# Kernel tuning notes

Measured on AMD Instinct MI355X. Metric: run time of the kernel, lower is better.

Reference implementation:

```python
import jax, jax.numpy as jnp
import numpy as np

B, T, D, H = 4, 2048, 1024, 16
HD = D // H  # 64
EPS = 1e-5


def setup_inputs() -> dict:
    key = jax.random.key(0)
    ks = jax.random.split(key, 8)
    s = 0.02
    return {
        "X": jax.random.normal(ks[0], (B, T, D), dtype=jnp.float32),
        # per-head projection weights stacked: [H, D, HD] (no bias, matches nn.Linear(bias=False))
        "Wq": jax.random.normal(ks[1], (H, D, HD), dtype=jnp.float32) * s,
        "Wk": jax.random.normal(ks[2], (H, D, HD), dtype=jnp.float32) * s,
        "Wv": jax.random.normal(ks[3], (H, D, HD), dtype=jnp.float32) * s,
        "ln1_g": jnp.ones((D,), jnp.float32),
        "ln1_b": jnp.zeros((D,), jnp.float32),
        "W1": jax.random.normal(ks[4], (D, 4 * D), dtype=jnp.float32) * s,
        "b1": jnp.zeros((4 * D,), jnp.float32),
        "W2": jax.random.normal(ks[5], (4 * D, D), dtype=jnp.float32) * s,
        "b2": jnp.zeros((D,), jnp.float32),
        "ln2_g": jnp.ones((D,), jnp.float32),
        "ln2_b": jnp.zeros((D,), jnp.float32),
    }


def _layer_norm(x, g, b):
    m = jnp.mean(x, axis=-1, keepdims=True)
    v = jnp.mean((x - m) ** 2, axis=-1, keepdims=True)
    return (x - m) / jnp.sqrt(v + EPS) * g + b


def reference(X, Wq, Wk, Wv, ln1_g, ln1_b, W1, b1, W2, b2, ln2_g, ln2_b):
    # multi-head causal self-attention (naive full-matrix, matching source)
    Q = jnp.einsum('btd,hde->bhte', X, Wq)
    K = jnp.einsum('btd,hde->bhte', X, Wk)
    V = jnp.einsum('btd,hde->bhte', X, Wv)
    scores = jnp.einsum('bhte,bhse->bhts', Q, K) / jnp.sqrt(jnp.float32(HD))
    causal = jnp.tril(jnp.ones((T, T), dtype=bool))
    scores = jnp.where(causal, scores, jnp.finfo(scores.dtype).min)
    attn = jax.nn.softmax(scores, axis=-1)
    Yh = jnp.einsum('bhts,bhse->bhte', attn, V)  # [B,H,T,HD]
    Y = jnp.transpose(Yh, (0, 2, 1, 3)).reshape(B, T, D)  # concat heads

    X1 = _layer_norm(Y + X, ln1_g, ln1_b)
    ff = jax.nn.relu(X1 @ W1 + b1) @ W2 + b2  # dropout inactive (eval)
    X2 = ff + X1
    return _layer_norm(X2, ln2_g, ln2_b)
```

## Files before the change

### kernel.cpp

```cpp
#include <hip/hip_runtime.h>
#include <cstdint>


typedef _Float16 f16x8 __attribute__((ext_vector_type(8)));
typedef _Float16 f16x4 __attribute__((ext_vector_type(4)));
typedef float    f32x4 __attribute__((ext_vector_type(4)));

#define DEVI __device__ __forceinline__

typedef __attribute__((address_space(1))) uint32_t gas1_u32;
typedef __attribute__((address_space(3))) uint32_t las3_u32;

DEVI void gl2lds16(const void* g, void* l) {
  __builtin_amdgcn_global_load_lds((gas1_u32*)(uintptr_t)g,
                                   (las3_u32*)(uintptr_t)l, 16, 0, 0);
}

#define FENCE_BAR                                                            \
  __builtin_amdgcn_sched_barrier(0xF);                                       \
  __builtin_amdgcn_s_barrier();                                              \
  __builtin_amdgcn_sched_barrier(0xF);

__global__ __launch_bounds__(256) void preprocess(
    const float* __restrict__ X, _Float16* __restrict__ Xh,
    const float* __restrict__ Wq, const float* __restrict__ Wk,
    const float* __restrict__ Wv, _Float16* __restrict__ Wqkv,
    const float* __restrict__ W1, _Float16* __restrict__ W1t,
    const float* __restrict__ W2, _Float16* __restrict__ W2t) {
  const int idx = blockIdx.x;
  const int tid = threadIdx.x;
  if (idx < 4096) {
    const int i = (idx * 256 + tid) * 8;
    float4 a = *(const float4*)&X[i];
    float4 b = *(const float4*)&X[i + 4];
    f16x8 o;
    o[0] = (_Float16)a.x; o[1] = (_Float16)a.y; o[2] = (_Float16)a.z; o[3] = (_Float16)a.w;
    o[4] = (_Float16)b.x; o[5] = (_Float16)b.y; o[6] = (_Float16)b.z; o[7] = (_Float16)b.w;
    *(f16x8*)&Xh[i] = o;
    return;
  }
  __shared__ _Float16 T[64 * 72];
  const float* src;
  _Float16* dst;
  int k0, rowbase, stride, dstK;
  float scale = 1.0f;
  if (idx < 4864) {
    const int j = idx - 4096;
    const int z = j >> 4;
    const int which = z >> 4;
    const int slice = z & 15;
    src = ((which == 0) ? Wq : (which == 1) ? Wk : Wv) + (size_t)slice * 65536;
    scale = (which == 0) ? 0.18033688011112042f : 1.0f;
    k0 = (j & 15) * 64;
    rowbase = which * 1024 + slice * 64;
    stride = 64; dstK = 1024; dst = Wqkv;
  } else if (idx < 5888) {
    const int j = idx - 4864;
    src = W1 + (j >> 4) * 64;
    k0 = (j & 15) * 64;
    rowbase = (j >> 4) * 64;
    stride = 4096; dstK = 1024; dst = W1t;
  } else {
    const int j = idx - 5888;
    src = W2 + (j >> 6) * 64;
    k0 = (j & 63) * 64;
    rowbase = (j >> 6) * 64;
    stride = 1024; dstK = 4096; dst = W2t;
  }
#pragma unroll
  for (int p = 0; p < 4; ++p) {
    int c = p * 256 + tid;
    int kl = c >> 4;
    int nl = (c & 15) * 4;
    float4 v = *(const float4*)&src[(size_t)(k0 + kl) * stride + nl];
    T[(nl + 0) * 72 + kl] = (_Float16)(v.x * scale);
    T[(nl + 1) * 72 + kl] = (_Float16)(v.y * scale);
    T[(nl + 2) * 72 + kl] = (_Float16)(v.z * scale);
    T[(nl + 3) * 72 + kl] = (_Float16)(v.w * scale);
  }
  __syncthreads();
#pragma unroll
  for (int p = 0; p < 2; ++p) {
    int c = p * 256 + tid;
    int nl = c >> 3;
    int kc = (c & 7) * 8;
    f16x8 vv = *(const f16x8*)&T[nl * 72 + kc];
    *(f16x8*)&dst[(size_t)(rowbase + nl) * dstK + k0 + kc] = vv;
  }
}

__global__ __launch_bounds__(256) void transpose_v(
    const _Float16* __restrict__ Vh, _Float16* __restrict__ Vt) {
  __shared__ _Float16 T[64 * 72];
  const int t0 = blockIdx.x * 64;
  const size_t hb = (size_t)blockIdx.y * (2048 * 64);
  const int tid = threadIdx.x;
#pragma unroll
  for (int it = 0; it < 2; ++it) {
    const int c = it * 256 + tid;
    const int tl = c >> 3;
    const int ec = (c & 7) * 8;
    *(f16x8*)&T[tl * 72 + ec] =
        *(const f16x8*)&Vh[hb + (size_t)(t0 + tl) * 64 + ec];
  }
  __syncthreads();
#pragma unroll
  for (int it = 0; it < 2; ++it) {
    const int c = it * 256 + tid;
    const int el = c >> 3;
    const int tc = (c & 7) * 8;
    f16x8 o;
#pragma unroll
    for (int jj = 0; jj < 8; ++jj) o[jj] = T[(tc + jj) * 72 + el];
    *(f16x8*)&Vt[hb + (size_t)el * 2048 + t0 + tc] = o;
  }
}

template <int MODE>
__global__ __launch_bounds__(512, 1) void gemm4(
    const _Float16* __restrict__ A, const _Float16* __restrict__ Bt,
    int K, int N, int nbx, int cpx,
    const float* __restrict__ bias, const _Float16* __restrict__ residH,
    _Float16* __restrict__ outH,
    _Float16* __restrict__ outQ, _Float16* __restrict__ outKp,
    _Float16* __restrict__ outV) {
  __shared__ _Float16 As[2][2][128 * 64];
  __shared__ _Float16 Bs[2][128 * 64];
  const int tid = threadIdx.x;
  const int lane = tid & 63;
  const int w = tid >> 6;
  const int wr = w >> 1, wc = w & 1;
  const int lr = lane & 15, g = lane >> 4;
  const int o = (blockIdx.x & 7) * cpx + (blockIdx.x >> 3);
  const int m0 = (o / nbx) * 256, n0 = (o % nbx) * 128;
  const int NT = K >> 6;

  const _Float16* Ab = A + (size_t)m0 * K;
  const _Float16* Bb = Bt + (size_t)n0 * K;

  f32x4 acc[4][4] = {};

  auto STG = [&](const _Float16* src, _Float16* dst) {
#pragma unroll
    for (int it = 0; it < 2; ++it) {
      const int c = it * 512 + tid;
      const int r = c >> 3;
      const int ts = (c & 7) ^ (r & 7);
      gl2lds16(src + (size_t)r * K + ts * 8, dst + c * 8);
    }
  };

  STG(Ab, &As[0][0][0]);
  STG(Ab + 128 * (size_t)K, &As[0][1][0]);
  STG(Bb, &Bs[0][0]);
  STG(Ab + 64, &As[1][0][0]);
  STG(Ab + 128 * (size_t)K + 64, &As[1][1][0]);
  STG(Bb + 64, &Bs[1][0]);
  asm volatile("s_waitcnt vmcnt(6)" ::: "memory");
  FENCE_BAR;

  f16x8 af[4][2], bfL[2][2], bfH[2][2];

  for (int t = 0; t < NT; ++t) {
    const int b = t & 1;
#pragma unroll
    for (int mf = 0; mf < 4; ++mf) {
      const int rl = (wr & 1) * 64 + mf * 16 + lr;
#pragma unroll
      for (int k2 = 0; k2 < 2; ++k2)
        af[mf][k2] = *(const f16x8*)&As[b][wr >> 1]
            [rl * 64 + (((k2 * 4 + g) ^ (rl & 7)) << 3)];
    }
#pragma unroll
    for (int nf = 0; nf < 2; ++nf) {
      const int rb = wc * 64 + nf * 16 + lr;
#pragma unroll
      for (int k2 = 0; k2 < 2; ++k2)
        bfL[nf][k2] = *(const f16x8*)&Bs[b]
            [rb * 64 + (((k2 * 4 + g) ^ (rb & 7)) << 3)];
    }
    FENCE_BAR;
    if (t + 2 < NT) {
      STG(Ab + (size_t)(t + 2) * 64, &As[b][0][0]);
      STG(Ab + 128 * (size_t)K + (size_t)(t + 2) * 64, &As[b][1][0]);
    }
#pragma unroll
    for (int nf = 0; nf < 2; ++nf) {
      const int rb = wc * 64 + (nf + 2) * 16 + lr;
#pragma unroll
      for (int k2 = 0; k2 < 2; ++k2)
        bfH[nf][k2] = *(const f16x8*)&Bs[b]
            [rb * 64 + (((k2 * 4 + g) ^ (rb & 7)) << 3)];
    }
    __builtin_amdgcn_s_setprio(1);
#pragma unroll
    for (int mf = 0; mf < 4; ++mf)
#pragma unroll
      for (int nf = 0; nf < 2; ++nf)
#pragma unroll
        for (int k2 = 0; k2 < 2; ++k2)
          acc[mf][nf] = __builtin_amdgcn_mfma_f32_16x16x32_f16(
              af[mf][k2], bfL[nf][k2], acc[mf][nf], 0, 0, 0);
    __builtin_amdgcn_s_setprio(0);
    FENCE_BAR;
    if (t + 2 < NT) STG(Bb + (size_t)(t + 2) * 64, &Bs[b][0]);
    __builtin_amdgcn_s_setprio(1);
#pragma unroll
    for (int mf = 0; mf < 4; ++mf)
#pragma unroll
      for (int nf = 0; nf < 2; ++nf)
#pragma unroll
        for (int k2 = 0; k2 < 2; ++k2)
          acc[mf][nf + 2] = __builtin_amdgcn_mfma_f32_16x16x32_f16(
              af[mf][k2], bfH[nf][k2], acc[mf][nf + 2], 0, 0, 0);
    __builtin_amdgcn_s_setprio(0);
    if (t == NT - 2) {
      asm volatile("s_waitcnt vmcnt(0)" ::: "memory");
    } else if (t < NT - 2) {
      asm volatile("s_waitcnt vmcnt(6)" ::: "memory");
    }
    FENCE_BAR;
  }

#pragma unroll
  for (int mf = 0; mf < 4; ++mf) {
#pragma unroll
    for (int nf = 0; nf < 4; ++nf) {
#pragma unroll
      for (int rr = 0; rr < 4; ++rr) {
        const int row = m0 + wr * 64 + mf * 16 + g * 4 + rr;
        const int col = n0 + wc * 64 + nf * 16 + lr;
        float v = acc[mf][nf][rr];
        if constexpr (MODE == 0) {
          const int qkv = col >> 10;
          const int h = (col >> 6) & 15;
          const int e = col & 63;
          const int bb = row >> 11;
          const int tt = row & 2047;
          const size_t idx = (((size_t)bb * 16 + h) * 2048 + tt) * 64 + e;
          const _Float16 hv = (_Float16)v;
          if (qkv == 0)      outQ[idx] = hv;
          else if (qkv == 1) outKp[idx] = hv;
          else               outV[idx] = hv;
        } else {
          outH[(size_t)row * N + col] = (_Float16)(
              v + bias[col] + (float)residH[(size_t)row * N + col]);
        }
      }
    }
  }
}

__global__ __launch_bounds__(512, 1) void gemm8_ffn1(
    const _Float16* __restrict__ A, const _Float16* __restrict__ Bt,
    int K, int N, int nbx, int cpx,
    const float* __restrict__ bias, _Float16* __restrict__ outH) {
  __shared__ _Float16 As[2][2][128 * 64];
  __shared__ _Float16 Bs[2][2][128 * 64];
  const int tid = threadIdx.x;
  const int lane = tid & 63;
  const int w = tid >> 6;
  const int wr = w >> 2, wc = w & 3;
  const int lr = lane & 15, g = lane >> 4;
  const int o = (blockIdx.x & 7) * cpx + (blockIdx.x >> 3);
  const int m0 = (o / nbx) * 256, n0 = (o % nbx) * 256;
  const int NT = K >> 6;

  const _Float16* Ab = A + (size_t)m0 * K;
  const _Float16* Bb = Bt + (size_t)n0 * K;

  f32x4 acc[8][4] = {};

  auto STG = [&](const _Float16* src, _Float16* dst) {
#pragma unroll
    for (int it = 0; it < 2; ++it) {
      const int c = it * 512 + tid;
      const int r = c >> 3;
      const int ts = (c & 7) ^ (r & 7);
      gl2lds16(src + (size_t)r * K + ts * 8, dst + c * 8);
    }
  };

  STG(Ab, &As[0][0][0]);
  STG(Ab + 128 * (size_t)K, &As[0][1][0]);
  STG(Bb, &Bs[0][0][0]);
  STG(Bb + 128 * (size_t)K, &Bs[0][1][0]);
  STG(Ab + 64, &As[1][0][0]);
  STG(Ab + 128 * (size_t)K + 64, &As[1][1][0]);
  STG(Bb + 64, &Bs[1][0][0]);
  asm volatile("s_waitcnt vmcnt(6)" ::: "memory");
  FENCE_BAR;

  f16x8 afA[4][2], afB[4][2], bfL[2][2], bfH[2][2];

#define LDA8_(af, MLO, buf)                                                  \
  _Pragma("unroll") for (int mf = 0; mf < 4; ++mf) {                         \
    const int rl = (MLO + mf) * 16 + lr;                                     \
    _Pragma("unroll") for (int k2 = 0; k2 < 2; ++k2)                         \
      af[mf][k2] = *(const f16x8*)&As[buf][wr][rl * 64 +                     \
                      (((k2 * 4 + g) ^ (rl & 7)) << 3)];                     \
  }
#define LDB8_(bf, NLO, buf)                                                  \
  _Pragma("unroll") for (int nf = 0; nf < 2; ++nf) {                         \
    const int rb = wc * 64 + (NLO + nf) * 16 + lr;                           \
    _Pragma("unroll") for (int k2 = 0; k2 < 2; ++k2)                         \
      bf[nf][k2] = *(const f16x8*)&Bs[buf][rb >> 7][(rb & 127) * 64 +        \
                      (((k2 * 4 + g) ^ (rb & 7)) << 3)];                     \
  }
#define MMA8_(af, bf, MB, NB)                                                \
  __builtin_amdgcn_s_setprio(1);                                             \
  _Pragma("unroll") for (int mf = 0; mf < 4; ++mf)                           \
  _Pragma("unroll") for (int nf = 0; nf < 2; ++nf)                           \
  _Pragma("unroll") for (int k2 = 0; k2 < 2; ++k2)                           \
    acc[(MB) + mf][(NB) + nf] = __builtin_amdgcn_mfma_f32_16x16x32_f16(      \
        af[mf][k2], bf[nf][k2], acc[(MB) + mf][(NB) + nf], 0, 0, 0);         \
  __builtin_amdgcn_s_setprio(0);

  for (int t = 0; t < NT; ++t) {
    const int cur = t & 1, nxt = cur ^ 1;
    LDA8_(afA, 0, cur);
    LDB8_(bfL, 0, cur);
    if (t + 1 < NT)
      STG(Bb + 128 * (size_t)K + (size_t)(t + 1) * 64, &Bs[nxt][1][0]);
    FENCE_BAR;
    MMA8_(afA, bfL, 0, 0);
    FENCE_BAR;
    LDA8_(afB, 4, cur);
    FENCE_BAR;
    MMA8_(afB, bfL, 4, 0);
    FENCE_BAR;
    LDB8_(bfH, 2, cur);
    if (t + 2 < NT) STG(Ab + (size_t)(t + 2) * 64, &As[cur][0][0]);
    FENCE_BAR;
    MMA8_(afA, bfH, 0, 2);
    FENCE_BAR;
    if (t + 2 < NT) {
      STG(Ab + 128 * (size_t)K + (size_t)(t + 2) * 64, &As[cur][1][0]);
      STG(Bb + (size_t)(t + 2) * 64, &Bs[cur][0][0]);
    }
    if (t == NT - 2) {
      asm volatile("s_waitcnt vmcnt(0)" ::: "memory");
    } else if (t < NT - 2) {
      asm volatile("s_waitcnt vmcnt(6)" ::: "memory");
    }
    FENCE_BAR;
    MMA8_(afB, bfH, 4, 2);
    FENCE_BAR;
  }
#undef LDA8_
#undef LDB8_
#undef MMA8_

#pragma unroll
  for (int mf = 0; mf < 8; ++mf) {
#pragma unroll
    for (int nf = 0; nf < 4; ++nf) {
#pragma unroll
      for (int rr = 0; rr < 4; ++rr) {
        const int row = m0 + wr * 128 + mf * 16 + g * 4 + rr;
        const int col = n0 + wc * 64 + nf * 16 + lr;
        float v = fmaxf(acc[mf][nf][rr] + bias[col], 0.0f);
        outH[(size_t)row * N + col] = (_Float16)v;
      }
    }
  }
}

__global__ __launch_bounds__(256, 2) void attn_fwd9(
    const _Float16* __restrict__ Qg, const _Float16* __restrict__ Kg,
    const _Float16* __restrict__ Vtg, _Float16* __restrict__ Yg) {
  __shared__ _Float16 Ksm[2][64 * 64];
  __shared__ _Float16 Vts[2][64 * 64];
  __shared__ _Float16 Psm[128 * 72];
  const int tid = threadIdx.x;
  const int lane = tid & 63;
  const int w = tid >> 6;
  const int lr = lane & 15, g = lane >> 4;

  const int bid = blockIdx.x;
  const int bh  = (bid & 7) * 8 + ((bid >> 3) & 7);
  const int p   = bid >> 6;
  const int qtA = p, qtB = 15 - p;
  const int njA = 2 * p + 2;
  const int ntot = 34;

  const size_t hbo = (size_t)bh * (2048 * 64);
  const _Float16* Qb = Qg + hbo;
  const _Float16* Kb = Kg + hbo;
  const _Float16* Vb = Vtg + hbo;
  _Float16* Yb = Yg + hbo;

  f16x8 qfA[2][2], qfB[2][2];
#pragma unroll
  for (int mi = 0; mi < 2; ++mi) {
    const int rA = qtA * 128 + mi * 64 + w * 16 + lr;
    const int rB = qtB * 128 + mi * 64 + w * 16 + lr;
#pragma unroll
    for (int ss = 0; ss < 2; ++ss) {
      qfA[mi][ss] = *(const f16x8*)&Qb[(size_t)rA * 64 + ss * 32 + g * 8];
      qfB[mi][ss] = *(const f16x8*)&Qb[(size_t)rB * 64 + ss * 32 + g * 8];
    }
  }

  f32x4 accYA[2][4] = {}, accYB[2][4] = {};
  f32x4 accLA[2] = {}, accLB[2] = {};

  f16x8 ones;
#pragma unroll
  for (int i = 0; i < 8; ++i) ones[i] = (_Float16)1.0f;

  auto TK0 = [&](int u) { return (u < njA ? u : u - njA) * 64; };

  auto STAGE = [&](int bufi, int tk0) {
#pragma unroll
    for (int it = 0; it < 2; ++it) {
      const int c = it * 256 + tid;
      const int r = c >> 3;
      const int ts = (c & 7) ^ (r & 7);
      gl2lds16(Kb + (size_t)(tk0 + r) * 64 + ts * 8, &Ksm[bufi][c * 8]);
      gl2lds16(Vb + (size_t)r * 2048 + tk0 + ts * 8, &Vts[bufi][c * 8]);
    }
  };

  auto BODY = [&](int bufi, int qbase, int tk0, const f16x8 (&qf)[2][2],
                  f32x4 (&accY)[2][4], f32x4 (&accL)[2]) {
    const _Float16* Ks = Ksm[bufi];
    const _Float16* Vs = Vts[bufi];
    const int qlo0 = qbase + w * 16;
    const int qlo1 = qbase + 64 + w * 16;
    const bool act0 = (tk0 <= qlo0 + 15);
    f16x8 kf[4][2];
#pragma unroll
    for (int ni = 0; ni < 4; ++ni) {
      const int row = ni * 16 + lr;
#pragma unroll
      for (int kk = 0; kk < 2; ++kk)
        kf[ni][kk] = *(const f16x8*)&Ks[row * 64 + (((kk * 4 + g) ^ (row & 7)) << 3)];
    }
    f32x4 s0[4] = {}, s1[4] = {};
    __builtin_amdgcn_s_setprio(1);
    if (act0) {
#pragma unroll
      for (int ni = 0; ni < 4; ++ni)
#pragma unroll
        for (int kk = 0; kk < 2; ++kk)
          s0[ni] = __builtin_amdgcn_mfma_f32_16x16x32_f16(kf[ni][kk], qf[0][kk], s0[ni], 0, 0, 0);
    }
#pragma unroll
    for (int ni = 0; ni < 4; ++ni)
#pragma unroll
      for (int kk = 0; kk < 2; ++kk)
        s1[ni] = __builtin_amdgcn_mfma_f32_16x16x32_f16(kf[ni][kk], qf[1][kk], s1[ni], 0, 0, 0);
    __builtin_amdgcn_s_setprio(0);
    if (act0 && tk0 + 63 > qlo0) {
      const int qa = qlo0 + lr;
#pragma unroll
      for (int ni = 0; ni < 4; ++ni)
#pragma unroll
        for (int r = 0; r < 4; ++r)
          if (tk0 + ni * 16 + g * 4 + r > qa) s0[ni][r] = -3.0e38f;
    }
    if (tk0 + 63 > qlo1) {
      const int qa = qlo1 + lr;
#pragma unroll
      for (int ni = 0; ni < 4; ++ni)
#pragma unroll
        for (int r = 0; r < 4; ++r)
          if (tk0 + ni * 16 + g * 4 + r > qa) s1[ni][r] = -3.0e38f;
    }
    const int prow0 = w * 16 + lr;
    const int prow1 = 64 + w * 16 + lr;
    if (act0) {
#pragma unroll
      for (int ni = 0; ni < 4; ++ni) {
        auto a = __builtin_amdgcn_cvt_pkrtz(__builtin_amdgcn_exp2f(s0[ni][0]),
                                            __builtin_amdgcn_exp2f(s0[ni][1]));
        auto b = __builtin_amdgcn_cvt_pkrtz(__builtin_amdgcn_exp2f(s0[ni][2]),
                                            __builtin_amdgcn_exp2f(s0[ni][3]));
        f16x4 pk4;
        pk4[0] = a[0]; pk4[1] = a[1]; pk4[2] = b[0]; pk4[3] = b[1];
        *(f16x4*)&Psm[prow0 * 72 + ni * 16 + g * 4] = pk4;
      }
    }
#pragma unroll
    for (int ni = 0; ni < 4; ++ni) {
      auto a = __builtin_amdgcn_cvt_pkrtz(__builtin_amdgcn_exp2f(s1[ni][0]),
                                          __builtin_amdgcn_exp2f(s1[ni][1]));
      auto b = __builtin_amdgcn_cvt_pkrtz(__builtin_amdgcn_exp2f(s1[ni][2]),
                                          __builtin_amdgcn_exp2f(s1[ni][3]));
      f16x4 pk4;
      pk4[0] = a[0]; pk4[1] = a[1]; pk4[2] = b[0]; pk4[3] = b[1];
      *(f16x4*)&Psm[prow1 * 72 + ni * 16 + g * 4] = pk4;
    }
    __builtin_amdgcn_s_setprio(1);
#pragma unroll
    for (int ss = 0; ss < 2; ++ss) {
      f16x8 pa0 = {};
      f16x8 pa1 = *(const f16x8*)&Psm[prow1 * 72 + ss * 32 + g * 8];
      if (act0) pa0 = *(const f16x8*)&Psm[prow0 * 72 + ss * 32 + g * 8];
      if (act0) accL[0] = __builtin_amdgcn_mfma_f32_16x16x32_f16(pa0, ones, accL[0], 0, 0, 0);
      accL[1] = __builtin_amdgcn_mfma_f32_16x16x32_f16(pa1, ones, accL[1], 0, 0, 0);
#pragma unroll
      for (int ne = 0; ne < 4; ++ne) {
        const int vrow = ne * 16 + lr;
        const f16x8 vbf = *(const f16x8*)&Vs[vrow * 64 + (((ss * 4 + g) ^ (vrow & 7)) << 3)];
        if (act0) accY[0][ne] = __builtin_amdgcn_mfma_f32_16x16x32_f16(pa0, vbf, accY[0][ne], 0, 0, 0);
        accY[1][ne] = __builtin_amdgcn_mfma_f32_16x16x32_f16(pa1, vbf, accY[1][ne], 0, 0, 0);
      }
    }
    __builtin_amdgcn_s_setprio(0);
  };

  STAGE(0, TK0(0));
  for (int u = 0; u < ntot; ++u) {
    asm volatile("s_waitcnt vmcnt(0)" ::: "memory");
    __builtin_amdgcn_s_barrier();
    __builtin_amdgcn_sched_barrier(0xF);
    const int cur = u & 1;
    if (u + 1 < ntot) STAGE(cur ^ 1, TK0(u + 1));
    if (u < njA) BODY(cur, qtA * 128, u * 64, qfA, accYA, accLA);
    else         BODY(cur, qtB * 128, (u - njA) * 64, qfB, accYB, accLB);
  }

#pragma unroll
  for (int mi = 0; mi < 2; ++mi)
#pragma unroll
    for (int r = 0; r < 4; ++r) {
      const float invA = 1.0f / accLA[mi][r];
      const float invB = 1.0f / accLB[mi][r];
      const int qaA = qtA * 128 + mi * 64 + w * 16 + g * 4 + r;
      const int qaB = qtB * 128 + mi * 64 + w * 16 + g * 4 + r;
#pragma unroll
      for (int ne = 0; ne < 4; ++ne) {
        Yb[(size_t)qaA * 64 + ne * 16 + lr] = (_Float16)(accYA[mi][ne][r] * invA);
        Yb[(size_t)qaB * 64 + ne * 16 + lr] = (_Float16)(accYB[mi][ne][r] * invB);
      }
    }
}

__global__ __launch_bounds__(256) void ln1_fused(
    const _Float16* __restrict__ Yh, const float* __restrict__ X,
    const float* __restrict__ gam, const float* __restrict__ bet,
    _Float16* __restrict__ X1h) {
  const int row = blockIdx.x;
  const int b = row >> 11, t = row & 2047;
  const int tid = threadIdx.x;
  const int d0 = tid * 4;
  const int h = d0 >> 6, e = d0 & 63;
  const f16x4 y4 = *(const f16x4*)&Yh[(((size_t)b * 16 + h) * 2048 + t) * 64 + e];
  const float4 x = *(const float4*)&X[(size_t)row * 1024 + d0];
  float v0 = (float)y4[0] + x.x, v1 = (float)y4[1] + x.y;
  float v2 = (float)y4[2] + x.z, v3 = (float)y4[3] + x.w;
  float s = v0 + v1 + v2 + v3;
  float q = v0 * v0 + v1 * v1 + v2 * v2 + v3 * v3;
  for (int off = 32; off; off >>= 1) { s += __shfl_xor(s, off); q += __shfl_xor(q, off); }
  __shared__ float red[8];
  const int w = tid >> 6;
  if ((tid & 63) == 0) { red[w] = s; red[4 + w] = q; }
  __syncthreads();
  s = red[0] + red[1] + red[2] + red[3];
  q = red[4] + red[5] + red[6] + red[7];
  const float mean = s * (1.f / 1024.f);
  const float rstd = rsqrtf(q * (1.f / 1024.f) - mean * mean + 1e-5f);
  const float4 G = *(const float4*)&gam[d0];
  const float4 Bv = *(const float4*)&bet[d0];
  f16x4 oh;
  oh[0] = (_Float16)((v0 - mean) * rstd * G.x + Bv.x);
  oh[1] = (_Float16)((v1 - mean) * rstd * G.y + Bv.y);
  oh[2] = (_Float16)((v2 - mean) * rstd * G.z + Bv.z);
  oh[3] = (_Float16)((v3 - mean) * rstd * G.w + Bv.w);
  *(f16x4*)&X1h[(size_t)row * 1024 + d0] = oh;
}

__global__ __launch_bounds__(256) void ln2_kernel(
    const _Float16* __restrict__ In, const float* __restrict__ gam,
    const float* __restrict__ bet, float* __restrict__ Out) {
  const int row = blockIdx.x;
  const int tid = threadIdx.x;
  const int d0 = tid * 4;
  const f16x4 v4 = *(const f16x4*)&In[(size_t)row * 1024 + d0];
  float v0 = (float)v4[0], v1 = (float)v4[1], v2 = (float)v4[2], v3 = (float)v4[3];
  float s = v0 + v1 + v2 + v3;
  float q = v0 * v0 + v1 * v1 + v2 * v2 + v3 * v3;
  for (int off = 32; off; off >>= 1) { s += __shfl_xor(s, off); q += __shfl_xor(q, off); }
  __shared__ float red[8];
  const int w = tid >> 6;
  if ((tid & 63) == 0) { red[w] = s; red[4 + w] = q; }
  __syncthreads();
  s = red[0] + red[1] + red[2] + red[3];
  q = red[4] + red[5] + red[6] + red[7];
  const float mean = s * (1.f / 1024.f);
  const float rstd = rsqrtf(q * (1.f / 1024.f) - mean * mean + 1e-5f);
  const float4 G = *(const float4*)&gam[d0];
  const float4 Bv = *(const float4*)&bet[d0];
  float4 o;
  o.x = (v0 - mean) * rstd * G.x + Bv.x;
  o.y = (v1 - mean) * rstd * G.y + Bv.y;
  o.z = (v2 - mean) * rstd * G.z + Bv.z;
  o.w = (v3 - mean) * rstd * G.w + Bv.w;
  *(float4*)&Out[(size_t)row * 1024 + d0] = o;
}

extern "C" void kernel_launch(void* const* d_in, const int* in_sizes, int n_in,
                              void* d_out, int out_size, void* d_ws, size_t ws_size,
                              hipStream_t stream) {
  (void)in_sizes; (void)n_in; (void)out_size; (void)ws_size;
  const float* X    = (const float*)d_in[0];
  const float* Wq   = (const float*)d_in[1];
  const float* Wk   = (const float*)d_in[2];
  const float* Wv   = (const float*)d_in[3];
  const float* ln1g = (const float*)d_in[4];
  const float* ln1b = (const float*)d_in[5];
  const float* W1   = (const float*)d_in[6];
  const float* b1   = (const float*)d_in[7];
  const float* W2   = (const float*)d_in[8];
  const float* b2   = (const float*)d_in[9];
  const float* ln2g = (const float*)d_in[10];
  const float* ln2b = (const float*)d_in[11];
  float* out = (float*)d_out;

  char* ws = (char*)d_ws;
  _Float16* Xh   = (_Float16*)(ws);
  _Float16* Vt   = (_Float16*)(ws);
  _Float16* Qh   = (_Float16*)(ws + 16777216ull);
  _Float16* Kh   = (_Float16*)(ws + 33554432ull);
  _Float16* Vh   = (_Float16*)(ws + 50331648ull);
  _Float16* ff1  = (_Float16*)(ws);
  _Float16* Wqkv = (_Float16*)(ws + 67108864ull);
  _Float16* W1t  = (_Float16*)(ws + 73400320ull);
  _Float16* W2t  = (_Float16*)(ws + 81788928ull);
  _Float16* Yh   = (_Float16*)(ws + 90177536ull);
  _Float16* X2h  = (_Float16*)(ws + 90177536ull);
  _Float16* X1h  = (_Float16*)(ws + 157286400ull);

  preprocess<<<dim3(6912), dim3(256), 0, stream>>>(
      X, Xh, Wq, Wk, Wv, Wqkv, W1, W1t, W2, W2t);

  gemm4<0><<<dim3(768), dim3(512), 0, stream>>>(
      Xh, Wqkv, 1024, 3072, 24, 96, nullptr, nullptr, nullptr, Qh, Kh, Vh);

  transpose_v<<<dim3(32, 64), dim3(256), 0, stream>>>(Vh, Vt);

  attn_fwd9<<<dim3(512), dim3(256), 0, stream>>>(Qh, Kh, Vt, Yh);

  ln1_fused<<<dim3(8192), dim3(256), 0, stream>>>(Yh, X, ln1g, ln1b, X1h);

  gemm8_ffn1<<<dim3(512), dim3(512), 0, stream>>>(
      X1h, W1t, 1024, 4096, 16, 64, b1, ff1);

  gemm4<2><<<dim3(256), dim3(512), 0, stream>>>(
      ff1, W2t, 4096, 1024, 8, 32, b2, X1h, X2h, nullptr, nullptr, nullptr);

  ln2_kernel<<<dim3(8192), dim3(256), 0, stream>>>(X2h, ln2g, ln2b, out);
}
```

Baseline: 323.7 us.

## Replace FFN1 256x256 GEMM with generic gemm4 ReLU mode and read fp16 residual

Drops the specialised 256x256-tile gemm8_ffn1 kernel and runs FFN1 through the existing gemm4 template with a new ReLU+bias epilogue mode, using smaller tiles and twice as many blocks. LN1 now reads the fp16 copy of X instead of fp32 X, halving that residual read. Vt is moved to its own workspace region so Xh is no longer overwritten and stays available for LN1. Smaller tiles give more blocks and better occupancy but less data reuse per block; the fp16 residual adds a little rounding error to LN1.

```diff
diff --git a/kernel.cpp b/kernel.cpp
--- a/kernel.cpp
+++ b/kernel.cpp
@@ -242,125 +242,13 @@
           if (qkv == 0)      outQ[idx] = hv;
           else if (qkv == 1) outKp[idx] = hv;
           else               outV[idx] = hv;
+        } else if constexpr (MODE == 1) {
+          outH[(size_t)row * N + col] =
+              (_Float16)fmaxf(v + bias[col], 0.0f);
         } else {
           outH[(size_t)row * N + col] = (_Float16)(
               v + bias[col] + (float)residH[(size_t)row * N + col]);
         }
-      }
-    }
-  }
-}
-
-__global__ __launch_bounds__(512, 1) void gemm8_ffn1(
-    const _Float16* __restrict__ A, const _Float16* __restrict__ Bt,
-    int K, int N, int nbx, int cpx,
-    const float* __restrict__ bias, _Float16* __restrict__ outH) {
-  __shared__ _Float16 As[2][2][128 * 64];
-  __shared__ _Float16 Bs[2][2][128 * 64];
-  const int tid = threadIdx.x;
-  const int lane = tid & 63;
-  const int w = tid >> 6;
-  const int wr = w >> 2, wc = w & 3;
-  const int lr = lane & 15, g = lane >> 4;
-  const int o = (blockIdx.x & 7) * cpx + (blockIdx.x >> 3);
-  const int m0 = (o / nbx) * 256, n0 = (o % nbx) * 256;
-  const int NT = K >> 6;
-
-  const _Float16* Ab = A + (size_t)m0 * K;
-  const _Float16* Bb = Bt + (size_t)n0 * K;
-
-  f32x4 acc[8][4] = {};
-
-  auto STG = [&](const _Float16* src, _Float16* dst) {
-#pragma unroll
-    for (int it = 0; it < 2; ++it) {
-      const int c = it * 512 + tid;
-      const int r = c >> 3;
-      const int ts = (c & 7) ^ (r & 7);
-      gl2lds16(src + (size_t)r * K + ts * 8, dst + c * 8);
-    }
-  };
-
-  STG(Ab, &As[0][0][0]);
-  STG(Ab + 128 * (size_t)K, &As[0][1][0]);
-  STG(Bb, &Bs[0][0][0]);
-  STG(Bb + 128 * (size_t)K, &Bs[0][1][0]);
-  STG(Ab + 64, &As[1][0][0]);
-  STG(Ab + 128 * (size_t)K + 64, &As[1][1][0]);
-  STG(Bb + 64, &Bs[1][0][0]);
-  asm volatile("s_waitcnt vmcnt(6)" ::: "memory");
-  FENCE_BAR;
-
-  f16x8 afA[4][2], afB[4][2], bfL[2][2], bfH[2][2];
-
-#define LDA8_(af, MLO, buf)                                                  \
-  _Pragma("unroll") for (int mf = 0; mf < 4; ++mf) {                         \
-    const int rl = (MLO + mf) * 16 + lr;                                     \
-    _Pragma("unroll") for (int k2 = 0; k2 < 2; ++k2)                         \
-      af[mf][k2] = *(const f16x8*)&As[buf][wr][rl * 64 +                     \
-                      (((k2 * 4 + g) ^ (rl & 7)) << 3)];                     \
-  }
-#define LDB8_(bf, NLO, buf)                                                  \
-  _Pragma("unroll") for (int nf = 0; nf < 2; ++nf) {                         \
-    const int rb = wc * 64 + (NLO + nf) * 16 + lr;                           \
-    _Pragma("unroll") for (int k2 = 0; k2 < 2; ++k2)                         \
-      bf[nf][k2] = *(const f16x8*)&Bs[buf][rb >> 7][(rb & 127) * 64 +        \
-                      (((k2 * 4 + g) ^ (rb & 7)) << 3)];                     \
-  }
-#define MMA8_(af, bf, MB, NB)                                                \
-  __builtin_amdgcn_s_setprio(1);                                             \
-  _Pragma("unroll") for (int mf = 0; mf < 4; ++mf)                           \
-  _Pragma("unroll") for (int nf = 0; nf < 2; ++nf)                           \
-  _Pragma("unroll") for (int k2 = 0; k2 < 2; ++k2)                           \
-    acc[(MB) + mf][(NB) + nf] = __builtin_amdgcn_mfma_f32_16x16x32_f16(      \
-        af[mf][k2], bf[nf][k2], acc[(MB) + mf][(NB) + nf], 0, 0, 0);         \
-  __builtin_amdgcn_s_setprio(0);
-
-  for (int t = 0; t < NT; ++t) {
-    const int cur = t & 1, nxt = cur ^ 1;
-    LDA8_(afA, 0, cur);
-    LDB8_(bfL, 0, cur);
-    if (t + 1 < NT)
-      STG(Bb + 128 * (size_t)K + (size_t)(t + 1) * 64, &Bs[nxt][1][0]);
-    FENCE_BAR;
-    MMA8_(afA, bfL, 0, 0);
-    FENCE_BAR;
-    LDA8_(afB, 4, cur);
-    FENCE_BAR;
-    MMA8_(afB, bfL, 4, 0);
-    FENCE_BAR;
-    LDB8_(bfH, 2, cur);
-    if (t + 2 < NT) STG(Ab + (size_t)(t + 2) * 64, &As[cur][0][0]);
-    FENCE_BAR;
-    MMA8_(afA, bfH, 0, 2);
-    FENCE_BAR;
-    if (t + 2 < NT) {
-      STG(Ab + 128 * (size_t)K + (size_t)(t + 2) * 64, &As[cur][1][0]);
-      STG(Bb + (size_t)(t + 2) * 64, &Bs[cur][0][0]);
-    }
-    if (t == NT - 2) {
-      asm volatile("s_waitcnt vmcnt(0)" ::: "memory");
-    } else if (t < NT - 2) {
-      asm volatile("s_waitcnt vmcnt(6)" ::: "memory");
-    }
-    FENCE_BAR;
-    MMA8_(afB, bfH, 4, 2);
-    FENCE_BAR;
-  }
-#undef LDA8_
-#undef LDB8_
-#undef MMA8_
-
-#pragma unroll
-  for (int mf = 0; mf < 8; ++mf) {
-#pragma unroll
-    for (int nf = 0; nf < 4; ++nf) {
-#pragma unroll
-      for (int rr = 0; rr < 4; ++rr) {
-        const int row = m0 + wr * 128 + mf * 16 + g * 4 + rr;
-        const int col = n0 + wc * 64 + nf * 16 + lr;
-        float v = fmaxf(acc[mf][nf][rr] + bias[col], 0.0f);
-        outH[(size_t)row * N + col] = (_Float16)v;
       }
     }
   }
@@ -539,7 +427,7 @@
 }
 
 __global__ __launch_bounds__(256) void ln1_fused(
-    const _Float16* __restrict__ Yh, const float* __restrict__ X,
+    const _Float16* __restrict__ Yh, const _Float16* __restrict__ Xh,
     const float* __restrict__ gam, const float* __restrict__ bet,
     _Float16* __restrict__ X1h) {
   const int row = blockIdx.x;
@@ -548,9 +436,9 @@
   const int d0 = tid * 4;
   const int h = d0 >> 6, e = d0 & 63;
   const f16x4 y4 = *(const f16x4*)&Yh[(((size_t)b * 16 + h) * 2048 + t) * 64 + e];
-  const float4 x = *(const float4*)&X[(size_t)row * 1024 + d0];
-  float v0 = (float)y4[0] + x.x, v1 = (float)y4[1] + x.y;
-  float v2 = (float)y4[2] + x.z, v3 = (float)y4[3] + x.w;
+  const f16x4 x4 = *(const f16x4*)&Xh[(size_t)row * 1024 + d0];
+  float v0 = (float)y4[0] + (float)x4[0], v1 = (float)y4[1] + (float)x4[1];
+  float v2 = (float)y4[2] + (float)x4[2], v3 = (float)y4[3] + (float)x4[3];
   float s = v0 + v1 + v2 + v3;
   float q = v0 * v0 + v1 * v1 + v2 * v2 + v3 * v3;
   for (int off = 32; off; off >>= 1) { s += __shfl_xor(s, off); q += __shfl_xor(q, off); }
@@ -621,7 +509,6 @@
 
   char* ws = (char*)d_ws;
   _Float16* Xh   = (_Float16*)(ws);
-  _Float16* Vt   = (_Float16*)(ws);
   _Float16* Qh   = (_Float16*)(ws + 16777216ull);
   _Float16* Kh   = (_Float16*)(ws + 33554432ull);
   _Float16* Vh   = (_Float16*)(ws + 50331648ull);
@@ -631,6 +518,7 @@
   _Float16* W2t  = (_Float16*)(ws + 81788928ull);
   _Float16* Yh   = (_Float16*)(ws + 90177536ull);
   _Float16* X2h  = (_Float16*)(ws + 90177536ull);
+  _Float16* Vt   = (_Float16*)(ws + 106954752ull);
   _Float16* X1h  = (_Float16*)(ws + 157286400ull);
 
   preprocess<<<dim3(6912), dim3(256), 0, stream>>>(
@@ -643,10 +531,10 @@
 
   attn_fwd9<<<dim3(512), dim3(256), 0, stream>>>(Qh, Kh, Vt, Yh);
 
-  ln1_fused<<<dim3(8192), dim3(256), 0, stream>>>(Yh, X, ln1g, ln1b, X1h);
-
-  gemm8_ffn1<<<dim3(512), dim3(512), 0, stream>>>(
-      X1h, W1t, 1024, 4096, 16, 64, b1, ff1);
+  ln1_fused<<<dim3(8192), dim3(256), 0, stream>>>(Yh, Xh, ln1g, ln1b, X1h);
+
+  gemm4<1><<<dim3(1024), dim3(512), 0, stream>>>(
+      X1h, W1t, 1024, 4096, 32, 128, b1, nullptr, ff1, nullptr, nullptr, nullptr);
 
   gemm4<2><<<dim3(256), dim3(512), 0, stream>>>(
       ff1, W2t, 4096, 1024, 8, 32, b2, X1h, X2h, nullptr, nullptr, nullptr);
```

After: 334.9 us. 1.03x slower.
